# Optimization experiments

Measured on AMD Instinct MI355X. Metric: run time of the kernel, lower is better.

Reference implementation:

```python
import jax, jax.numpy as jnp
import numpy as np

N, F_IN, H, MH = 50000, 128, 128, 256
E = 800000

def _lin_init(key, out_d, in_d, bias=True):
    k1, k2 = jax.random.split(key)
    bound = 1.0 / np.sqrt(in_d)
    W = jax.random.uniform(k1, (out_d, in_d), minval=-bound, maxval=bound, dtype=jnp.float32)
    if bias:
        b = jax.random.uniform(k2, (out_d,), minval=-bound, maxval=bound, dtype=jnp.float32)
        return W, b
    return W, None

def setup_inputs() -> dict:
    key = jax.random.key(0)
    ks = jax.random.split(key, 8)
    x = jax.random.normal(ks[0], (N, F_IN), dtype=jnp.float32)
    edge_index = jax.random.randint(ks[1], (2, E), 0, N, dtype=jnp.int64)
    W1l, b1l = _lin_init(ks[2], H, F_IN, bias=True)   # SAGEConv1 neighbor lin (with bias)
    W1r, _ = _lin_init(ks[3], H, F_IN, bias=False)    # SAGEConv1 root lin (no bias)
    W2l, b2l = _lin_init(ks[4], H, H, bias=True)
    W2r, _ = _lin_init(ks[5], H, H, bias=False)
    Wm1, bm1 = _lin_init(ks[6], MH, 2 * H, bias=True)
    Wm2, bm2 = _lin_init(ks[7], 1, MH, bias=True)
    return {"x": x, "edge_index": edge_index,
            "W1l": W1l, "b1l": b1l, "W1r": W1r,
            "W2l": W2l, "b2l": b2l, "W2r": W2r,
            "Wm1": Wm1, "bm1": bm1, "Wm2": Wm2, "bm2": bm2}

def _sage_conv(x, src, dst, Wl, bl, Wr, num_nodes):
    # mean-aggregate messages x[src] at dst, then lin_l(agg) + lin_r(x)
    agg = jax.ops.segment_sum(x[src], dst, num_segments=num_nodes)
    cnt = jax.ops.segment_sum(jnp.ones((src.shape[0],), x.dtype), dst, num_segments=num_nodes)
    agg = agg / jnp.maximum(cnt, 1.0)[:, None]
    return agg @ Wl.T + bl + x @ Wr.T

def reference(x, edge_index, W1l, b1l, W1r, W2l, b2l, W2r, Wm1, bm1, Wm2, bm2):
    src, dst = edge_index[0], edge_index[1]
    n = x.shape[0]
    h = jax.nn.relu(_sage_conv(x, src, dst, W1l, b1l, W1r, n))
    # dropout is identity in eval mode
    h = jax.nn.relu(_sage_conv(h, src, dst, W2l, b2l, W2r, n))
    ef = jnp.concatenate([h[src], h[dst]], axis=-1)  # [E, 2H]
    out = jax.nn.relu(ef @ Wm1.T + bm1) @ Wm2.T + bm2
    return out.reshape(-1)
```

## Files before the change

### kernel.cpp

```cpp
#include <hip/hip_runtime.h>
#include <hip/hip_bf16.h>

#define NN 50000
#define F 128
#define EE 800000
#define MHD 256

typedef __attribute__((ext_vector_type(8))) short bf16x8;
typedef __attribute__((ext_vector_type(4))) float f32x4;

__device__ __forceinline__ float b2f(unsigned short u) {
    union { unsigned int i; float f; } v; v.i = ((unsigned)u) << 16; return v.f;
}
__device__ __forceinline__ unsigned short f2b(float f) {
    unsigned int x = __float_as_uint(f);
    unsigned int r = x + 0x7fffu + ((x >> 16) & 1u);
    return (unsigned short)(r >> 16);
}

__global__ __launch_bounds__(256) void cast_x_kernel(
    const float* __restrict__ in, unsigned short* __restrict__ out) {
    int i = (blockIdx.x * 256 + threadIdx.x) * 4;
    float4 v = *(const float4*)(in + i);
    ushort4 o; o.x = f2b(v.x); o.y = f2b(v.y); o.z = f2b(v.z); o.w = f2b(v.w);
    *(ushort4*)(out + i) = o;
}

__global__ __launch_bounds__(256) void cast_w_kernel(
    const float* __restrict__ W1l, const float* __restrict__ W1r,
    const float* __restrict__ W2l, const float* __restrict__ W2r,
    const float* __restrict__ Wm1, unsigned short* __restrict__ wb) {
    int i = (blockIdx.x * 256 + threadIdx.x) * 4;
    unsigned short o[4];
    if (i < 32768) {
        const float* p = (i < 16384) ? (W1l + i) : (W1r + (i - 16384));
        float4 v = *(const float4*)p;
        o[0] = f2b(v.x); o[1] = f2b(v.y); o[2] = f2b(v.z); o[3] = f2b(v.w);
    } else if (i < 65536) {
        int local = i - 32768;
        const float* M = (local < 16384) ? W2l : W2r;
        int lm = local & 16383;
        int n = lm >> 7, kp = lm & 127;
#pragma unroll
        for (int t = 0; t < 4; t++) {
            int k = ((kp + t) & 7) * 16 + ((kp + t) >> 3);
            o[t] = f2b(M[n * 128 + k]);
        }
    } else {
        int local = i - 65536;
        int n = local >> 8, k2 = local & 255;
        int half = k2 >> 7, kp = k2 & 127;
#pragma unroll
        for (int t = 0; t < 4; t++) {
            int k = half * 128 + ((kp + t) & 7) * 16 + ((kp + t) >> 3);
            o[t] = f2b(Wm1[n * 256 + k]);
        }
    }
    *(ushort4*)(wb + i) = *(ushort4*)o;
}

__global__ __launch_bounds__(256) void edge_cvt_hist_kernel(
    const int* __restrict__ ei, int* __restrict__ s32, int* __restrict__ d32,
    int* __restrict__ deg) {
    __shared__ int isI64;
    if (threadIdx.x == 0) {
        int z = 0;
        for (int i = 1; i < 128; i += 2) z |= ei[i];
        isI64 = (z == 0) ? 1 : 0;
    }
    __syncthreads();
    int e = blockIdx.x * 256 + threadIdx.x;
    if (e >= EE) return;
    int s, d;
    if (isI64) {
        const long long* e64 = (const long long*)ei;
        s = (int)e64[e];
        d = (int)e64[EE + e];
    } else {
        s = ei[e];
        d = ei[EE + e];
    }
    s32[e] = s;
    d32[e] = d;
    atomicAdd(&deg[d], 1);
}

__global__ __launch_bounds__(1024) void scan_p1_kernel(
    const int* __restrict__ deg, int* __restrict__ exloc, int* __restrict__ bsum) {
    __shared__ int part[1024];
    int t = threadIdx.x, gid = blockIdx.x * 1024 + t;
    int v = (gid < NN) ? deg[gid] : 0;
    part[t] = v;
    __syncthreads();
    for (int off = 1; off < 1024; off <<= 1) {
        int u = (t >= off) ? part[t - off] : 0;
        __syncthreads();
        part[t] += u;
        __syncthreads();
    }
    exloc[gid] = part[t] - v;
    if (t == 1023) bsum[blockIdx.x] = part[t];
}

__global__ __launch_bounds__(1024) void scan_p3_kernel(
    const int* __restrict__ exloc, const int* __restrict__ bsum,
    int* __restrict__ rowstart, int* __restrict__ cursor) {
    __shared__ int offs;
    if (threadIdx.x == 0) {
        int s = 0;
        for (int b = 0; b < blockIdx.x; b++) s += bsum[b];
        offs = s;
    }
    __syncthreads();
    int gid = blockIdx.x * 1024 + threadIdx.x;
    if (gid > NN) return;
    if (gid == NN) { rowstart[NN] = EE; return; }
    int r = exloc[gid] + offs;
    rowstart[gid] = r;
    cursor[gid] = r;
}

__global__ __launch_bounds__(256) void fill_kernel(
    const int* __restrict__ s32, const int* __restrict__ d32,
    int* __restrict__ cursor, int* __restrict__ nbr, int* __restrict__ eid) {
    int e = blockIdx.x * 256 + threadIdx.x;
    if (e < EE) {
        int p = atomicAdd(&cursor[d32[e]], 1);
        nbr[p] = s32[e];
        eid[p] = e;
    }
}

__global__ __launch_bounds__(256) void sage_layer_kernel(
    const unsigned short* __restrict__ xin,
    const int* __restrict__ nbr, const int* __restrict__ rowstart,
    const unsigned short* __restrict__ W1, const unsigned short* __restrict__ W2,
    const float* __restrict__ bias,
    unsigned short* __restrict__ out) {
    __shared__ unsigned short lds[4][16][136];
    int wave = threadIdx.x >> 6, lane = threadIdx.x & 63;
    int m0 = (blockIdx.x * 4 + wave) * 16;

    int g = lane >> 4, l16 = lane & 15, col8 = l16 * 8;
    for (int batch = 0; batch < 4; batch++) {
        int node = m0 + batch * 4 + g;
        int beg = 0, end = 0;
        if (node < NN) { beg = rowstart[node]; end = rowstart[node + 1]; }
        float a[8] = {0,0,0,0,0,0,0,0};
        int j = beg;
        for (; j + 3 < end; j += 4) {
            int s0 = nbr[j], s1 = nbr[j + 1], s2 = nbr[j + 2], s3 = nbr[j + 3];
            bf16x8 v0 = *(const bf16x8*)(xin + (size_t)s0 * F + col8);
            bf16x8 v1 = *(const bf16x8*)(xin + (size_t)s1 * F + col8);
            bf16x8 v2 = *(const bf16x8*)(xin + (size_t)s2 * F + col8);
            bf16x8 v3 = *(const bf16x8*)(xin + (size_t)s3 * F + col8);
            for (int i = 0; i < 8; i++)
                a[i] += (b2f((unsigned short)v0[i]) + b2f((unsigned short)v1[i]))
                      + (b2f((unsigned short)v2[i]) + b2f((unsigned short)v3[i]));
        }
        for (; j < end; j++) {
            int s0 = nbr[j];
            bf16x8 v0 = *(const bf16x8*)(xin + (size_t)s0 * F + col8);
            for (int i = 0; i < 8; i++) a[i] += b2f((unsigned short)v0[i]);
        }
        float inv = 1.0f / fmaxf((float)(end - beg), 1.0f);
        unsigned short o[8];
        for (int i = 0; i < 8; i++) o[i] = f2b(a[i] * inv);
        *(bf16x8*)&lds[wave][batch * 4 + g][col8] = *(bf16x8*)o;
    }
    __syncthreads();

    int c = lane & 15, q = lane >> 4;
    f32x4 acc[8];
    for (int nt = 0; nt < 8; nt++) {
        float b = bias[nt * 16 + c];
        acc[nt] = (f32x4){b, b, b, b};
    }
    int mrow = m0 + c; if (mrow > NN - 1) mrow = NN - 1;
    for (int op = 0; op < 2; op++) {
        const unsigned short* W = op ? W2 : W1;
        for (int kb = 0; kb < 4; kb++) {
            bf16x8 a;
            if (op == 0) a = *(const bf16x8*)&lds[wave][c][kb * 32 + q * 8];
            else         a = *(const bf16x8*)(xin + (size_t)mrow * F + kb * 32 + q * 8);
            for (int nt = 0; nt < 8; nt++) {
                bf16x8 b = *(const bf16x8*)(W + (size_t)(nt * 16 + c) * F + kb * 32 + q * 8);
                acc[nt] = __builtin_amdgcn_mfma_f32_16x16x32_bf16(a, b, acc[nt], 0, 0, 0);
            }
        }
    }
#pragma unroll
    for (int r = 0; r < 4; r++) {
        int node = m0 + q * 4 + r;
        if (node < NN) {
            unsigned short o[8];
#pragma unroll
            for (int nt = 0; nt < 8; nt++) o[nt] = f2b(fmaxf(acc[nt][r], 0.0f));
            *(bf16x8*)(out + (size_t)node * F + c * 8) = *(bf16x8*)o;
        }
    }
}

__global__ __launch_bounds__(256) void pq_gemm_kernel(
    const unsigned short* __restrict__ h,
    const unsigned short* __restrict__ wmb,
    const float* __restrict__ bm1,
    unsigned short* __restrict__ PQ) {
    int wave = threadIdx.x >> 6, lane = threadIdx.x & 63;
    int c = lane & 15, q = lane >> 4;
    int half = wave >> 1, ntBase = (wave & 1) * 8;
    int m0 = blockIdx.x * 16;
    int mrow = m0 + c; if (mrow > NN - 1) mrow = NN - 1;
    bf16x8 a[4];
#pragma unroll
    for (int kb = 0; kb < 4; kb++)
        a[kb] = *(const bf16x8*)(h + (size_t)mrow * F + kb * 32 + q * 8);
    f32x4 acc[8];
#pragma unroll
    for (int nt = 0; nt < 8; nt++) {
        float b = half ? bm1[(ntBase + nt) * 16 + c] : 0.0f;
        acc[nt] = (f32x4){b, b, b, b};
    }
#pragma unroll
    for (int kb = 0; kb < 4; kb++) {
#pragma unroll
        for (int nt = 0; nt < 8; nt++) {
            bf16x8 b = *(const bf16x8*)(wmb + (size_t)((ntBase + nt) * 16 + c) * 256 + half * 128 + kb * 32 + q * 8);
            acc[nt] = __builtin_amdgcn_mfma_f32_16x16x32_bf16(a[kb], b, acc[nt], 0, 0, 0);
        }
    }
#pragma unroll
    for (int r = 0; r < 4; r++) {
        int node = m0 + q * 4 + r;
        if (node < NN) {
            unsigned short o[8];
#pragma unroll
            for (int nt = 0; nt < 8; nt++) o[nt] = f2b(acc[nt][r]);
            *(bf16x8*)(PQ + (size_t)node * 512 + half * 256 + c * 16 + ntBase) = *(bf16x8*)o;
        }
    }
}

__global__ __launch_bounds__(256) void edge_dot_kernel(
    const unsigned short* __restrict__ PQ,
    const int* __restrict__ nbr, const int* __restrict__ eid,
    const int* __restrict__ rowstart,
    const float* __restrict__ Wm2, const float* __restrict__ bm2,
    float* __restrict__ out) {
    int wave = threadIdx.x >> 6, lane = threadIdx.x & 63;
    int node = blockIdx.x * 4 + wave;
    if (node >= NN) return;
    int g = lane >> 4, l16 = lane & 15;
    int col = l16 * 16;
    float w2f[16], qf[16];
#pragma unroll
    for (int i = 0; i < 16; i++) w2f[i] = Wm2[i * 16 + l16];
    {
        bf16x8 q0 = *(const bf16x8*)(PQ + (size_t)node * 512 + 256 + col);
        bf16x8 q1 = *(const bf16x8*)(PQ + (size_t)node * 512 + 256 + col + 8);
#pragma unroll
        for (int i = 0; i < 8; i++) { qf[i] = b2f((unsigned short)q0[i]); qf[8 + i] = b2f((unsigned short)q1[i]); }
    }
    float b2 = bm2[0];
    int beg = rowstart[node], end = rowstart[node + 1];
    int j = beg + g;
    for (; j + 4 < end; j += 8) {
        int s0 = nbr[j], s1 = nbr[j + 4];
        int id0 = eid[j], id1 = eid[j + 4];
        uint4 a0 = *(const uint4*)(PQ + (size_t)s0 * 512 + col);
        uint4 a1 = *(const uint4*)(PQ + (size_t)s0 * 512 + col + 8);
        uint4 c0 = *(const uint4*)(PQ + (size_t)s1 * 512 + col);
        uint4 c1 = *(const uint4*)(PQ + (size_t)s1 * 512 + col + 8);
        float t0 = 0.f, t1 = 0.f;
        unsigned int w0[8] = {a0.x, a0.y, a0.z, a0.w, a1.x, a1.y, a1.z, a1.w};
        unsigned int w1[8] = {c0.x, c0.y, c0.z, c0.w, c1.x, c1.y, c1.z, c1.w};
#pragma unroll
        for (int i = 0; i < 8; i++) {
            float lo0 = __uint_as_float(w0[i] << 16);
            float hi0 = __uint_as_float(w0[i] & 0xffff0000u);
            float lo1 = __uint_as_float(w1[i] << 16);
            float hi1 = __uint_as_float(w1[i] & 0xffff0000u);
            t0 += fmaxf(lo0 + qf[2 * i], 0.f) * w2f[2 * i]
                + fmaxf(hi0 + qf[2 * i + 1], 0.f) * w2f[2 * i + 1];
            t1 += fmaxf(lo1 + qf[2 * i], 0.f) * w2f[2 * i]
                + fmaxf(hi1 + qf[2 * i + 1], 0.f) * w2f[2 * i + 1];
        }
        t0 += __shfl_xor(t0, 1);  t1 += __shfl_xor(t1, 1);
        t0 += __shfl_xor(t0, 2);  t1 += __shfl_xor(t1, 2);
        t0 += __shfl_xor(t0, 4);  t1 += __shfl_xor(t1, 4);
        t0 += __shfl_xor(t0, 8);  t1 += __shfl_xor(t1, 8);
        if (l16 == 0) { out[id0] = t0 + b2; out[id1] = t1 + b2; }
    }
    for (; j < end; j += 4) {
        int s = nbr[j];
        int id = eid[j];
        uint4 a0 = *(const uint4*)(PQ + (size_t)s * 512 + col);
        uint4 a1 = *(const uint4*)(PQ + (size_t)s * 512 + col + 8);
        unsigned int w0[8] = {a0.x, a0.y, a0.z, a0.w, a1.x, a1.y, a1.z, a1.w};
        float t = 0.f;
#pragma unroll
        for (int i = 0; i < 8; i++) {
            float lo = __uint_as_float(w0[i] << 16);
            float hi = __uint_as_float(w0[i] & 0xffff0000u);
            t += fmaxf(lo + qf[2 * i], 0.f) * w2f[2 * i]
               + fmaxf(hi + qf[2 * i + 1], 0.f) * w2f[2 * i + 1];
        }
        t += __shfl_xor(t, 1);
        t += __shfl_xor(t, 2);
        t += __shfl_xor(t, 4);
        t += __shfl_xor(t, 8);
        if (l16 == 0) out[id] = t + b2;
    }
}

extern "C" void kernel_launch(void* const* d_in, const int* in_sizes, int n_in,
                              void* d_out, int out_size, void* d_ws, size_t ws_size,
                              hipStream_t stream) {
    const float* x   = (const float*)d_in[0];
    const int*   ei  = (const int*)d_in[1];
    const float* W1l = (const float*)d_in[2];
    const float* b1l = (const float*)d_in[3];
    const float* W1r = (const float*)d_in[4];
    const float* W2l = (const float*)d_in[5];
    const float* b2l = (const float*)d_in[6];
    const float* W2r = (const float*)d_in[7];
    const float* Wm1 = (const float*)d_in[8];
    const float* bm1 = (const float*)d_in[9];
    const float* Wm2 = (const float*)d_in[10];
    const float* bm2 = (const float*)d_in[11];

    char* ws = (char*)d_ws;
    unsigned short* PQ       = (unsigned short*)(ws);
    unsigned short* xb       = (unsigned short*)(ws);
    unsigned short* h1       = (unsigned short*)(ws + 12800000);
    unsigned short* wb       = (unsigned short*)(ws + 51200000);
    int*            s32      = (int*)(ws + 51462144);
    int*            d32      = (int*)(ws + 54662144);
    int*            deg      = (int*)(ws + 57862144);
    int*            rowstart = (int*)(ws + 58062208);
    int*            cursor   = (int*)(ws + 58262272);
    int*            nbr      = (int*)(ws + 58462336);
    int*            eid      = (int*)(ws + 61662336);
    unsigned short* h2       = (unsigned short*)(ws + 64862336);
    int*            exloc    = (int*)(ws + 77662336);
    int*            bsum     = (int*)(ws + 77867136);
    float*          outp     = (float*)d_out;

    const unsigned short* w1l_b  = wb;
    const unsigned short* w1r_b  = wb + 16384;
    const unsigned short* w2l_p  = wb + 32768;
    const unsigned short* w2r_p  = wb + 49152;
    const unsigned short* wm1_p  = wb + 65536;

    cast_x_kernel<<<6250, 256, 0, stream>>>(x, xb);
    cast_w_kernel<<<128, 256, 0, stream>>>(W1l, W1r, W2l, W2r, Wm1, wb);
    hipMemsetAsync(deg, 0, 200064, stream);
    edge_cvt_hist_kernel<<<3125, 256, 0, stream>>>(ei, s32, d32, deg);
    scan_p1_kernel<<<50, 1024, 0, stream>>>(deg, exloc, bsum);
    scan_p3_kernel<<<50, 1024, 0, stream>>>(exloc, bsum, rowstart, cursor);
    fill_kernel<<<3125, 256, 0, stream>>>(s32, d32, cursor, nbr, eid);

    sage_layer_kernel<<<782, 256, 0, stream>>>(xb, nbr, rowstart, w1l_b, w1r_b, b1l, h1);
    sage_layer_kernel<<<782, 256, 0, stream>>>(h1, nbr, rowstart, w2l_p, w2r_p, b2l, h2);
    pq_gemm_kernel<<<3125, 256, 0, stream>>>(h2, wm1_p, bm1, PQ);
    edge_dot_kernel<<<12500, 256, 0, stream>>>(PQ, nbr, eid, rowstart, Wm2, bm2, outp);
}
```

Measured before the change: 434.3 us.

## Fuse cast/memset launches, interleave neighbor and edge ids, unroll gather by eight

Merges the x cast, weight cast and degree memset into one kernel launch to cut launch overhead. Stores neighbor source and edge id as an interleaved int2 array so each CSR entry is fetched with one load. Adds an 8-way unrolled gather loop with two accumulator sets in the SAGE aggregation to keep more loads in flight. The int2 layout doubles the bytes read in the SAGE layers, which only need the source id.

Measured after the change: 424.5 us (median of 2 runs). 2.3% less time.

```diff
diff --git a/kernel.cpp b/kernel.cpp
--- a/kernel.cpp
+++ b/kernel.cpp
@@ -18,45 +18,51 @@
     return (unsigned short)(r >> 16);
 }
 
-__global__ __launch_bounds__(256) void cast_x_kernel(
-    const float* __restrict__ in, unsigned short* __restrict__ out) {
-    int i = (blockIdx.x * 256 + threadIdx.x) * 4;
-    float4 v = *(const float4*)(in + i);
-    ushort4 o; o.x = f2b(v.x); o.y = f2b(v.y); o.z = f2b(v.z); o.w = f2b(v.w);
-    *(ushort4*)(out + i) = o;
-}
-
-__global__ __launch_bounds__(256) void cast_w_kernel(
+__global__ __launch_bounds__(256) void cast_zero_kernel(
+    const float* __restrict__ x,
     const float* __restrict__ W1l, const float* __restrict__ W1r,
     const float* __restrict__ W2l, const float* __restrict__ W2r,
-    const float* __restrict__ Wm1, unsigned short* __restrict__ wb) {
-    int i = (blockIdx.x * 256 + threadIdx.x) * 4;
-    unsigned short o[4];
-    if (i < 32768) {
-        const float* p = (i < 16384) ? (W1l + i) : (W1r + (i - 16384));
-        float4 v = *(const float4*)p;
-        o[0] = f2b(v.x); o[1] = f2b(v.y); o[2] = f2b(v.z); o[3] = f2b(v.w);
-    } else if (i < 65536) {
-        int local = i - 32768;
-        const float* M = (local < 16384) ? W2l : W2r;
-        int lm = local & 16383;
-        int n = lm >> 7, kp = lm & 127;
-#pragma unroll
-        for (int t = 0; t < 4; t++) {
-            int k = ((kp + t) & 7) * 16 + ((kp + t) >> 3);
-            o[t] = f2b(M[n * 128 + k]);
-        }
+    const float* __restrict__ Wm1,
+    unsigned short* __restrict__ xb, unsigned short* __restrict__ wb,
+    int* __restrict__ deg) {
+    int bid = blockIdx.x;
+    if (bid < 6250) {
+        int i = (bid * 256 + threadIdx.x) * 4;
+        float4 v = *(const float4*)(x + i);
+        ushort4 o; o.x = f2b(v.x); o.y = f2b(v.y); o.z = f2b(v.z); o.w = f2b(v.w);
+        *(ushort4*)(xb + i) = o;
+    } else if (bid < 6378) {
+        int i = ((bid - 6250) * 256 + threadIdx.x) * 4;
+        unsigned short o[4];
+        if (i < 32768) {
+            const float* p = (i < 16384) ? (W1l + i) : (W1r + (i - 16384));
+            float4 v = *(const float4*)p;
+            o[0] = f2b(v.x); o[1] = f2b(v.y); o[2] = f2b(v.z); o[3] = f2b(v.w);
+        } else if (i < 65536) {
+            int local = i - 32768;
+            const float* M = (local < 16384) ? W2l : W2r;
+            int lm = local & 16383;
+            int n = lm >> 7, kp = lm & 127;
+#pragma unroll
+            for (int t = 0; t < 4; t++) {
+                int k = ((kp + t) & 7) * 16 + ((kp + t) >> 3);
+                o[t] = f2b(M[n * 128 + k]);
+            }
+        } else {
+            int local = i - 65536;
+            int n = local >> 8, k2 = local & 255;
+            int half = k2 >> 7, kp = k2 & 127;
+#pragma unroll
+            for (int t = 0; t < 4; t++) {
+                int k = half * 128 + ((kp + t) & 7) * 16 + ((kp + t) >> 3);
+                o[t] = f2b(Wm1[n * 256 + k]);
+            }
+        }
+        *(ushort4*)(wb + i) = *(ushort4*)o;
     } else {
-        int local = i - 65536;
-        int n = local >> 8, k2 = local & 255;
-        int half = k2 >> 7, kp = k2 & 127;
-#pragma unroll
-        for (int t = 0; t < 4; t++) {
-            int k = half * 128 + ((kp + t) & 7) * 16 + ((kp + t) >> 3);
-            o[t] = f2b(Wm1[n * 256 + k]);
-        }
-    }
-    *(ushort4*)(wb + i) = *(ushort4*)o;
+        int idx = ((bid - 6378) * 256 + threadIdx.x) * 4;
+        if (idx < 50016) *(int4*)(deg + idx) = (int4){0, 0, 0, 0};
+    }
 }
 
 __global__ __launch_bounds__(256) void edge_cvt_hist_kernel(
@@ -122,18 +128,17 @@
 
 __global__ __launch_bounds__(256) void fill_kernel(
     const int* __restrict__ s32, const int* __restrict__ d32,
-    int* __restrict__ cursor, int* __restrict__ nbr, int* __restrict__ eid) {
+    int* __restrict__ cursor, int2* __restrict__ nedge) {
     int e = blockIdx.x * 256 + threadIdx.x;
     if (e < EE) {
         int p = atomicAdd(&cursor[d32[e]], 1);
-        nbr[p] = s32[e];
-        eid[p] = e;
+        nedge[p] = make_int2(s32[e], e);
     }
 }
 
 __global__ __launch_bounds__(256) void sage_layer_kernel(
     const unsigned short* __restrict__ xin,
-    const int* __restrict__ nbr, const int* __restrict__ rowstart,
+    const int2* __restrict__ nedge, const int* __restrict__ rowstart,
     const unsigned short* __restrict__ W1, const unsigned short* __restrict__ W2,
     const float* __restrict__ bias,
     unsigned short* __restrict__ out) {
@@ -147,9 +152,28 @@
         int beg = 0, end = 0;
         if (node < NN) { beg = rowstart[node]; end = rowstart[node + 1]; }
         float a[8] = {0,0,0,0,0,0,0,0};
+        float b[8] = {0,0,0,0,0,0,0,0};
         int j = beg;
+        for (; j + 7 < end; j += 8) {
+            int s0 = nedge[j].x,     s1 = nedge[j + 1].x, s2 = nedge[j + 2].x, s3 = nedge[j + 3].x;
+            int s4 = nedge[j + 4].x, s5 = nedge[j + 5].x, s6 = nedge[j + 6].x, s7 = nedge[j + 7].x;
+            bf16x8 v0 = *(const bf16x8*)(xin + (size_t)s0 * F + col8);
+            bf16x8 v1 = *(const bf16x8*)(xin + (size_t)s1 * F + col8);
+            bf16x8 v2 = *(const bf16x8*)(xin + (size_t)s2 * F + col8);
+            bf16x8 v3 = *(const bf16x8*)(xin + (size_t)s3 * F + col8);
+            bf16x8 v4 = *(const bf16x8*)(xin + (size_t)s4 * F + col8);
+            bf16x8 v5 = *(const bf16x8*)(xin + (size_t)s5 * F + col8);
+            bf16x8 v6 = *(const bf16x8*)(xin + (size_t)s6 * F + col8);
+            bf16x8 v7 = *(const bf16x8*)(xin + (size_t)s7 * F + col8);
+            for (int i = 0; i < 8; i++)
+                a[i] += (b2f((unsigned short)v0[i]) + b2f((unsigned short)v1[i]))
+                      + (b2f((unsigned short)v2[i]) + b2f((unsigned short)v3[i]));
+            for (int i = 0; i < 8; i++)
+                b[i] += (b2f((unsigned short)v4[i]) + b2f((unsigned short)v5[i]))
+                      + (b2f((unsigned short)v6[i]) + b2f((unsigned short)v7[i]));
+        }
         for (; j + 3 < end; j += 4) {
-            int s0 = nbr[j], s1 = nbr[j + 1], s2 = nbr[j + 2], s3 = nbr[j + 3];
+            int s0 = nedge[j].x, s1 = nedge[j + 1].x, s2 = nedge[j + 2].x, s3 = nedge[j + 3].x;
             bf16x8 v0 = *(const bf16x8*)(xin + (size_t)s0 * F + col8);
             bf16x8 v1 = *(const bf16x8*)(xin + (size_t)s1 * F + col8);
             bf16x8 v2 = *(const bf16x8*)(xin + (size_t)s2 * F + col8);
@@ -159,13 +183,13 @@
                       + (b2f((unsigned short)v2[i]) + b2f((unsigned short)v3[i]));
         }
         for (; j < end; j++) {
-            int s0 = nbr[j];
+            int s0 = nedge[j].x;
             bf16x8 v0 = *(const bf16x8*)(xin + (size_t)s0 * F + col8);
             for (int i = 0; i < 8; i++) a[i] += b2f((unsigned short)v0[i]);
         }
         float inv = 1.0f / fmaxf((float)(end - beg), 1.0f);
         unsigned short o[8];
-        for (int i = 0; i < 8; i++) o[i] = f2b(a[i] * inv);
+        for (int i = 0; i < 8; i++) o[i] = f2b((a[i] + b[i]) * inv);
         *(bf16x8*)&lds[wave][batch * 4 + g][col8] = *(bf16x8*)o;
     }
     __syncthreads();
@@ -243,8 +267,7 @@
 
 __global__ __launch_bounds__(256) void edge_dot_kernel(
     const unsigned short* __restrict__ PQ,
-    const int* __restrict__ nbr, const int* __restrict__ eid,
-    const int* __restrict__ rowstart,
+    const int2* __restrict__ nedge, const int* __restrict__ rowstart,
     const float* __restrict__ Wm2, const float* __restrict__ bm2,
     float* __restrict__ out) {
     int wave = threadIdx.x >> 6, lane = threadIdx.x & 63;
@@ -265,12 +288,11 @@
     int beg = rowstart[node], end = rowstart[node + 1];
     int j = beg + g;
     for (; j + 4 < end; j += 8) {
-        int s0 = nbr[j], s1 = nbr[j + 4];
-        int id0 = eid[j], id1 = eid[j + 4];
-        uint4 a0 = *(const uint4*)(PQ + (size_t)s0 * 512 + col);
-        uint4 a1 = *(const uint4*)(PQ + (size_t)s0 * 512 + col + 8);
-        uint4 c0 = *(const uint4*)(PQ + (size_t)s1 * 512 + col);
-        uint4 c1 = *(const uint4*)(PQ + (size_t)s1 * 512 + col + 8);
+        int2 e0 = nedge[j], e1 = nedge[j + 4];
+        uint4 a0 = *(const uint4*)(PQ + (size_t)e0.x * 512 + col);
+        uint4 a1 = *(const uint4*)(PQ + (size_t)e0.x * 512 + col + 8);
+        uint4 c0 = *(const uint4*)(PQ + (size_t)e1.x * 512 + col);
+        uint4 c1 = *(const uint4*)(PQ + (size_t)e1.x * 512 + col + 8);
         float t0 = 0.f, t1 = 0.f;
         unsigned int w0[8] = {a0.x, a0.y, a0.z, a0.w, a1.x, a1.y, a1.z, a1.w};
         unsigned int w1[8] = {c0.x, c0.y, c0.z, c0.w, c1.x, c1.y, c1.z, c1.w};
@@ -289,13 +311,12 @@
         t0 += __shfl_xor(t0, 2);  t1 += __shfl_xor(t1, 2);
         t0 += __shfl_xor(t0, 4);  t1 += __shfl_xor(t1, 4);
         t0 += __shfl_xor(t0, 8);  t1 += __shfl_xor(t1, 8);
-        if (l16 == 0) { out[id0] = t0 + b2; out[id1] = t1 + b2; }
+        if (l16 == 0) { out[e0.y] = t0 + b2; out[e1.y] = t1 + b2; }
     }
     for (; j < end; j += 4) {
-        int s = nbr[j];
-        int id = eid[j];
-        uint4 a0 = *(const uint4*)(PQ + (size_t)s * 512 + col);
-        uint4 a1 = *(const uint4*)(PQ + (size_t)s * 512 + col + 8);
+        int2 e0 = nedge[j];
+        uint4 a0 = *(const uint4*)(PQ + (size_t)e0.x * 512 + col);
+        uint4 a1 = *(const uint4*)(PQ + (size_t)e0.x * 512 + col + 8);
         unsigned int w0[8] = {a0.x, a0.y, a0.z, a0.w, a1.x, a1.y, a1.z, a1.w};
         float t = 0.f;
 #pragma unroll
@@ -309,7 +330,7 @@
         t += __shfl_xor(t, 2);
         t += __shfl_xor(t, 4);
         t += __shfl_xor(t, 8);
-        if (l16 == 0) out[id] = t + b2;
+        if (l16 == 0) out[e0.y] = t + b2;
     }
 }
 
@@ -339,8 +360,7 @@
     int*            deg      = (int*)(ws + 57862144);
     int*            rowstart = (int*)(ws + 58062208);
     int*            cursor   = (int*)(ws + 58262272);
-    int*            nbr      = (int*)(ws + 58462336);
-    int*            eid      = (int*)(ws + 61662336);
+    int2*           nedge    = (int2*)(ws + 58462336);
     unsigned short* h2       = (unsigned short*)(ws + 64862336);
     int*            exloc    = (int*)(ws + 77662336);
     int*            bsum     = (int*)(ws + 77867136);
@@ -352,16 +372,14 @@
     const unsigned short* w2r_p  = wb + 49152;
     const unsigned short* wm1_p  = wb + 65536;
 
-    cast_x_kernel<<<6250, 256, 0, stream>>>(x, xb);
-    cast_w_kernel<<<128, 256, 0, stream>>>(W1l, W1r, W2l, W2r, Wm1, wb);
-    hipMemsetAsync(deg, 0, 200064, stream);
+    cast_zero_kernel<<<6427, 256, 0, stream>>>(x, W1l, W1r, W2l, W2r, Wm1, xb, wb, deg);
     edge_cvt_hist_kernel<<<3125, 256, 0, stream>>>(ei, s32, d32, deg);
     scan_p1_kernel<<<50, 1024, 0, stream>>>(deg, exloc, bsum);
     scan_p3_kernel<<<50, 1024, 0, stream>>>(exloc, bsum, rowstart, cursor);
-    fill_kernel<<<3125, 256, 0, stream>>>(s32, d32, cursor, nbr, eid);
-
-    sage_layer_kernel<<<782, 256, 0, stream>>>(xb, nbr, rowstart, w1l_b, w1r_b, b1l, h1);
-    sage_layer_kernel<<<782, 256, 0, stream>>>(h1, nbr, rowstart, w2l_p, w2r_p, b2l, h2);
+    fill_kernel<<<3125, 256, 0, stream>>>(s32, d32, cursor, nedge);
+
+    sage_layer_kernel<<<782, 256, 0, stream>>>(xb, nedge, rowstart, w1l_b, w1r_b, b1l, h1);
+    sage_layer_kernel<<<782, 256, 0, stream>>>(h1, nedge, rowstart, w2l_p, w2r_p, b2l, h2);
     pq_gemm_kernel<<<3125, 256, 0, stream>>>(h2, wm1_p, bm1, PQ);
-    edge_dot_kernel<<<12500, 256, 0, stream>>>(PQ, nbr, eid, rowstart, Wm2, bm2, outp);
-}
+    edge_dot_kernel<<<12500, 256, 0, stream>>>(PQ, nedge, rowstart, Wm2, bm2, outp);
+}
```
